# Kernel tuning notes

Hardware: AMD Instinct MI355X
Metric: run time of the kernel (lower is better)

The kernel has to match this reference:

```python
import jax, jax.numpy as jnp
import numpy as np

EPS = 1e-5        # torch BatchNorm2d default eps
G = 8             # DCNv4 groups
KP = 9            # 3x3 kernel points


def conv2d(x, w):
    return jax.lax.conv_general_dilated(
        x, w, window_strides=(1, 1), padding='SAME',
        dimension_numbers=('NCHW', 'OIHW', 'NCHW'))


def bn_eval(x, g_, b_, m_, v_):
    s = g_ / jnp.sqrt(v_ + EPS)
    return x * s[None, :, None, None] + (b_ - m_ * s)[None, :, None, None]


def silu(x):
    return x * jax.nn.sigmoid(x)


def dcnv4_core(value, offset, mask):
    # value: (N,H,W,G,Cg)  offset: (N,H,W,G,K,2) (x,y)  mask: (N,H,W,G,K) unnormalized (DCNv4: no softmax)
    N, H, W, Gn, Cg = value.shape
    r = jnp.arange(-1, 2, dtype=value.dtype)              # dilation=1, pad=1, 3x3 grid
    gy, gx = jnp.meshgrid(r, r, indexing='ij')
    grid_x = gx.ravel()  # (9,)
    grid_y = gy.ravel()
    px = jnp.arange(W, dtype=value.dtype)[None, None, :, None, None] + grid_x + offset[..., 0]
    py = jnp.arange(H, dtype=value.dtype)[None, :, None, None, None] + grid_y + offset[..., 1]
    x0 = jnp.floor(px); y0 = jnp.floor(py)
    lx = px - x0; ly = py - y0
    x0i = x0.astype(jnp.int32); y0i = y0.astype(jnp.int32)
    bidx = jnp.arange(N)[:, None, None, None, None]
    gidx = jnp.arange(Gn)[None, None, None, :, None]

    def tap(yi, xi, wgt):
        valid = (yi >= 0) & (yi < H) & (xi >= 0) & (xi < W)   # zero padding outside
        v = value[bidx, jnp.clip(yi, 0, H - 1), jnp.clip(xi, 0, W - 1), gidx]  # (N,H,W,G,K,Cg)
        return v * (wgt * valid)[..., None]

    s = (tap(y0i, x0i, (1 - ly) * (1 - lx))
         + tap(y0i, x0i + 1, (1 - ly) * lx)
         + tap(y0i + 1, x0i, ly * (1 - lx))
         + tap(y0i + 1, x0i + 1, ly * lx))
    return jnp.einsum('nhwgkc,nhwgk->nhwgc', s, mask)


def dcnv4(x, val_w, val_b, om_w, om_b, outp_w, outp_b):
    # x: NCHW. DCNv4 wrapper: flatten to tokens, value_proj, offset_mask linear on raw tokens,
    # deformable aggregation, output_proj, back to NCHW.
    N, C, H, W = x.shape
    t = x.transpose(0, 2, 3, 1).reshape(N, H * W, C)
    value = (t @ val_w.T + val_b).reshape(N, H, W, G, C // G)
    om = (t @ om_w.T + om_b).reshape(N, H, W, G, KP * 3)  # per group: 2K offsets then K masks
    offset = om[..., :2 * KP].reshape(N, H, W, G, KP, 2)
    mask = om[..., 2 * KP:]
    out = dcnv4_core(value, offset, mask).reshape(N, H * W, C)
    out = out @ outp_w.T + outp_b
    return out.reshape(N, H, W, C).transpose(0, 3, 1, 2)


def setup_inputs() -> dict:
    key = jax.random.key(0)
    ks = jax.random.split(key, 32)
    W_SC = 0.05
    d = {}
    d['x'] = jax.random.normal(ks[0], (4, 256, 64, 64), jnp.float32)
    d['cv1_w'] = jax.random.normal(ks[1], (128, 256, 3, 3), jnp.float32) * W_SC
    d['cv1_bn_g'] = jax.random.uniform(ks[2], (128,), jnp.float32, 0.5, 1.5)
    d['cv1_bn_b'] = jax.random.normal(ks[3], (128,), jnp.float32) * 0.1
    d['cv1_bn_m'] = jax.random.normal(ks[4], (128,), jnp.float32) * 0.1
    d['cv1_bn_v'] = jax.random.uniform(ks[5], (128,), jnp.float32, 0.5, 1.5)
    d['cv2_w'] = jax.random.normal(ks[6], (256, 128, 3, 3), jnp.float32) * W_SC
    d['cv2_bn_g'] = jax.random.uniform(ks[7], (256,), jnp.float32, 0.5, 1.5)
    d['cv2_bn_b'] = jax.random.normal(ks[8], (256,), jnp.float32) * 0.1
    d['cv2_bn_m'] = jax.random.normal(ks[9], (256,), jnp.float32) * 0.1
    d['cv2_bn_v'] = jax.random.uniform(ks[10], (256,), jnp.float32, 0.5, 1.5)
    d['val_w'] = jax.random.normal(ks[11], (256, 256), jnp.float32) * W_SC
    d['val_b'] = jax.random.normal(ks[12], (256,), jnp.float32) * 0.01
    d['om_w'] = jax.random.normal(ks[13], (216, 256), jnp.float32) * 0.02
    d['om_b'] = jax.random.normal(ks[14], (216,), jnp.float32) * 0.01
    d['outp_w'] = jax.random.normal(ks[15], (256, 256), jnp.float32) * W_SC
    d['outp_b'] = jax.random.normal(ks[16], (256,), jnp.float32) * 0.01
    d['bn3_g'] = jax.random.uniform(ks[17], (256,), jnp.float32, 0.5, 1.5)
    d['bn3_b'] = jax.random.normal(ks[18], (256,), jnp.float32) * 0.1
    d['bn3_m'] = jax.random.normal(ks[19], (256,), jnp.float32) * 0.1
    d['bn3_v'] = jax.random.uniform(ks[20], (256,), jnp.float32, 0.5, 1.5)
    d['pw1_w'] = jax.random.normal(ks[21], (768, 256, 1, 1), jnp.float32) * W_SC
    d['pw1_b'] = jax.random.normal(ks[22], (768,), jnp.float32) * 0.01
    d['pw2_w'] = jax.random.normal(ks[23], (256, 768, 1, 1), jnp.float32) * W_SC
    d['pw2_b'] = jax.random.normal(ks[24], (256,), jnp.float32) * 0.01
    return d


def reference(x, cv1_w, cv1_bn_g, cv1_bn_b, cv1_bn_m, cv1_bn_v,
              cv2_w, cv2_bn_g, cv2_bn_b, cv2_bn_m, cv2_bn_v,
              val_w, val_b, om_w, om_b, outp_w, outp_b,
              bn3_g, bn3_b, bn3_m, bn3_v, pw1_w, pw1_b, pw2_w, pw2_b):
    # cv2(cv1(x)) branch: Conv = Conv2d(no bias) + BN + SiLU
    y = silu(bn_eval(conv2d(x, cv1_w), cv1_bn_g, cv1_bn_b, cv1_bn_m, cv1_bn_v))
    y = silu(bn_eval(conv2d(y, cv2_w), cv2_bn_g, cv2_bn_b, cv2_bn_m, cv2_bn_v))
    # dcn branch: DCNv4 -> BN -> 1x1 conv (+SiLU) -> 1x1 conv
    d = dcnv4(x, val_w, val_b, om_w, om_b, outp_w, outp_b)
    d = bn_eval(d, bn3_g, bn3_b, bn3_m, bn3_v)
    d = silu(conv2d(d, pw1_w) + pw1_b[None, :, None, None])
    d = conv2d(d, pw2_w) + pw2_b[None, :, None, None]
    return x + y + d
```

## Files before the change

### kernel.cpp

```cpp
#include <hip/hip_runtime.h>
#include <math.h>

typedef __attribute__((ext_vector_type(8))) __bf16 bf16x8;
typedef __attribute__((ext_vector_type(8))) unsigned short us8;
typedef __attribute__((ext_vector_type(4))) unsigned short us4;
typedef __attribute__((ext_vector_type(4))) float f32x4;
typedef __attribute__((ext_vector_type(4))) int i32x4;
typedef unsigned int uint32;

#define EPSV 1e-5f

__device__ __forceinline__ float silu_f(float v) { return v / (1.f + __expf(-v)); }

__device__ __forceinline__ unsigned short f2bf(float f) {
  uint32 u = __builtin_bit_cast(uint32, f);
  u += 0x7fffu + ((u >> 16) & 1u);
  return (unsigned short)(u >> 16);
}
__device__ __forceinline__ float bf2f(unsigned short h) {
  uint32 u = ((uint32)h) << 16;
  return __builtin_bit_cast(float, u);
}

__device__ __forceinline__ void gl_lds16(const void* g, void* l) {
  __builtin_amdgcn_global_load_lds(
      (const __attribute__((address_space(1))) unsigned int*)g,
      (__attribute__((address_space(3))) unsigned int*)l, 16, 0, 0);
}

template <int EPI, int CIN, int BN>
__device__ __forceinline__ void gemm_body(
    int rb, int cb, int k0, int KL,
    const unsigned short* __restrict__ A, const unsigned short* __restrict__ Bw,
    const float* __restrict__ bias, int K, int Co, void* __restrict__ outv,
    const float* __restrict__ e0, const float* __restrict__ e1,
    const float* __restrict__ e2, const float* __restrict__ e3,
    const unsigned short* __restrict__ zpage, bf16x8* smem) {
  constexpr int NFR = BN / 32;
  constexpr int NB = BN / 64;
  constexpr int CPB = 512 + BN * 4;
  const int t = threadIdx.x;
  const int lane = t & 63;
  const int wv = t >> 6;
  const int wr = wv >> 1, wc = wv & 1;

  f32x4 acc[4][NFR];
#pragma unroll
  for (int i = 0; i < 4; i++)
#pragma unroll
    for (int j = 0; j < NFR; j++) acc[i][j] = (f32x4){0.f, 0.f, 0.f, 0.f};

  const unsigned short* Abase[2];
  int aprow[2], apcol[2], akoff[2];
#pragma unroll
  for (int i = 0; i < 2; i++) {
    int c = t + 256 * i;
    int row = (c >> 6) * 16 + (c & 15);
    int koff = ((c >> 4) & 3) * 8;
    akoff[i] = koff;
    int grow = rb + row;
    if constexpr (CIN > 0) {
      int n = grow >> 12, p = grow & 4095;
      aprow[i] = p >> 6;
      apcol[i] = p & 63;
      Abase[i] = A + (size_t)n * 4096 * CIN;
    } else {
      Abase[i] = A + (size_t)grow * K + koff;
    }
  }
  const unsigned short* Bbase[NB];
#pragma unroll
  for (int i = 0; i < NB; i++) {
    int c = t + 256 * i;
    int col = cb + (c >> 6) * 16 + (c & 15);
    int koff = ((c >> 4) & 3) * 8;
    Bbase[i] = (col < Co) ? (Bw + (size_t)col * K + koff) : zpage;
  }
  auto addrA = [&](int i, int kb) -> const unsigned short* {
    if constexpr (CIN > 0) {
      int tap = kb / CIN;
      int ci = (kb & (CIN - 1)) + akoff[i];
      int dy = tap / 3 - 1, dx = tap % 3 - 1;
      int h = aprow[i] + dy, w = apcol[i] + dx;
      if (((unsigned)h < 64u) & ((unsigned)w < 64u))
        return &Abase[i][(size_t)(h * 64 + w) * CIN + ci];
      return zpage;
    } else {
      return Abase[i] + kb;
    }
  };
  auto stage = [&](int buf, int kb) {
    bf16x8* base = &smem[buf * CPB];
    gl_lds16(addrA(0, kb), (void*)&base[t]);
    gl_lds16(addrA(1, kb), (void*)&base[t + 256]);
    gl_lds16((Bbase[0] == zpage) ? zpage : Bbase[0] + kb, (void*)&base[512 + t]);
    if constexpr (NB == 2)
      gl_lds16((Bbase[1] == zpage) ? zpage : Bbase[1] + kb,
               (void*)&base[512 + t + 256]);
  };

  const int nt = KL >> 5;
  stage(0, k0);
  __syncthreads();
  int cur = 0;
  for (int it = 0; it < nt; ++it) {
    if (it + 1 < nt) stage(cur ^ 1, k0 + ((it + 1) << 5));
    const bf16x8* Ab = &smem[cur * CPB];
    const bf16x8* Bb = Ab + 512;
    bf16x8 af[4], bfr[NFR];
#pragma unroll
    for (int mi = 0; mi < 4; mi++) af[mi] = Ab[(wr * 4 + mi) * 64 + lane];
#pragma unroll
    for (int ni = 0; ni < NFR; ni++) bfr[ni] = Bb[(wc * NFR + ni) * 64 + lane];
    __builtin_amdgcn_s_setprio(1);
#pragma unroll
    for (int mi = 0; mi < 4; mi++)
#pragma unroll
      for (int ni = 0; ni < NFR; ni++)
        acc[mi][ni] = __builtin_amdgcn_mfma_f32_16x16x32_bf16(af[mi], bfr[ni],
                                                              acc[mi][ni], 0, 0, 0);
    __builtin_amdgcn_s_setprio(0);
    __syncthreads();
    cur ^= 1;
  }

  const int lr = lane & 15, kg4 = (lane >> 4) * 4;
#pragma unroll
  for (int mi = 0; mi < 4; mi++) {
#pragma unroll
    for (int ni = 0; ni < NFR; ni++) {
      int gcol = cb + wc * (BN / 2) + ni * 16 + lr;
      if (gcol >= Co) continue;
      float bval, s = 1.f, tt = 0.f;
      if (EPI == 2 || EPI == 7) bval = 0.f;
      else if (EPI == 5) bval = (gcol < 256) ? bias[gcol] : e0[gcol - 256];
      else bval = bias[gcol];
      if (EPI == 2 || EPI == 3) {
        s = e0[gcol] * rsqrtf(e3[gcol] + EPSV);
        tt = e1[gcol] - e2[gcol] * s;
      }
      if (EPI == 6) {
        int grow0 = rb + wr * 64 + mi * 16 + kg4;
        int n = grow0 >> 12, p0 = grow0 & 4095;
        size_t oix = ((size_t)(n * 256 + gcol)) * 4096 + p0;
        f32x4 xv = *(const f32x4*)&((const float*)e0)[oix];
        const unsigned short* y2p = (const unsigned short*)e1;
        f32x4 ov;
#pragma unroll
        for (int j = 0; j < 4; j++) {
          float y2 = bf2f(y2p[((size_t)(n * 4096 + p0 + j)) * 256 + gcol]);
          ov[j] = acc[mi][ni][j] + bval + xv[j] + y2;
        }
        *(f32x4*)&((float*)outv)[oix] = ov;
        continue;
      }
#pragma unroll
      for (int j = 0; j < 4; j++) {
        int grow = rb + wr * 64 + mi * 16 + kg4 + j;
        float v = acc[mi][ni][j] + bval;
        if (EPI == 2) v = silu_f(v * s + tt);
        if (EPI == 3) v = v * s + tt;
        if (EPI == 4) v = silu_f(v);
        if (EPI == 5) {
          if (gcol < 256)
            ((unsigned short*)outv)[(size_t)grow * 256 + gcol] = f2bf(v);
          else
            ((float*)e1)[(size_t)grow * 216 + (gcol - 256)] = v;
        } else {
          ((unsigned short*)outv)[(size_t)grow * Co + gcol] = f2bf(v);
        }
      }
    }
  }
}

__device__ __forceinline__ void dcn_body(
    int bid, const unsigned short* __restrict__ value,
    const float* __restrict__ om, unsigned short* __restrict__ out,
    void* smemraw) {
  f32x4* wgt = (f32x4*)smemraw;
  i32x4* adr = (i32x4*)((char*)smemraw + 576 * 16);
  const int n = bid >> 9;
  const int p0 = (bid & 511) * 8;
  const int t = threadIdx.x;

  for (int idx = t; idx < 576; idx += 256) {
    int pi = idx / 72;
    int gk = idx - pi * 72;
    int g = gk / 9, k = gk - g * 9;
    int p = p0 + pi;
    int h0 = p >> 6, w0 = p & 63;
    const float* omp = om + ((size_t)(n * 4096 + p)) * 216 + g * 27;
    float ox = omp[2 * k], oy = omp[2 * k + 1], mk = omp[18 + k];
    float px = (float)(w0 + (k % 3) - 1) + ox;
    float py = (float)(h0 + (k / 3) - 1) + oy;
    float x0f = floorf(px), y0f = floorf(py);
    float lx = px - x0f, ly = py - y0f;
    int x0 = (int)x0f, y0 = (int)y0f;
    int x1 = x0 + 1, y1 = y0 + 1;
    bool vx0 = (unsigned)x0 < 64u, vx1 = (unsigned)x1 < 64u;
    bool vy0 = (unsigned)y0 < 64u, vy1 = (unsigned)y1 < 64u;
    int cx0 = min(max(x0, 0), 63), cx1 = min(max(x1, 0), 63);
    int cy0 = min(max(y0, 0), 63), cy1 = min(max(y1, 0), 63);
    f32x4 w4;
    w4[0] = (1.f - ly) * (1.f - lx) * mk * (float)(vy0 && vx0);
    w4[1] = (1.f - ly) * lx * mk * (float)(vy0 && vx1);
    w4[2] = ly * (1.f - lx) * mk * (float)(vy1 && vx0);
    w4[3] = ly * lx * mk * (float)(vy1 && vx1);
    i32x4 a4;
    a4[0] = (cy0 * 64 + cx0) * 256;
    a4[1] = (cy0 * 64 + cx1) * 256;
    a4[2] = (cy1 * 64 + cx0) * 256;
    a4[3] = (cy1 * 64 + cx1) * 256;
    wgt[idx] = w4;
    adr[idx] = a4;
  }
  __syncthreads();

  const int pi = t >> 5;
  const int g = (t >> 2) & 7;
  const int l = t & 3;
  const int p = p0 + pi;
  const unsigned short* vb = value + ((size_t)n * 4096) * 256 + g * 32 + l * 8;
  const int bix = (pi * 8 + g) * 9;
  float a[8] = {0.f, 0.f, 0.f, 0.f, 0.f, 0.f, 0.f, 0.f};
#pragma unroll
  for (int k = 0; k < 9; k++) {
    f32x4 wv = wgt[bix + k];
    i32x4 av = adr[bix + k];
    us8 q0 = *(const us8*)(vb + av[0]);
    us8 q1 = *(const us8*)(vb + av[1]);
    us8 q2 = *(const us8*)(vb + av[2]);
    us8 q3 = *(const us8*)(vb + av[3]);
#pragma unroll
    for (int j = 0; j < 8; j++)
      a[j] += wv[0] * bf2f(q0[j]) + wv[1] * bf2f(q1[j]) +
              wv[2] * bf2f(q2[j]) + wv[3] * bf2f(q3[j]);
  }
  us8 o;
#pragma unroll
  for (int j = 0; j < 8; j++) o[j] = f2bf(a[j]);
  *(us8*)&out[((size_t)(n * 4096 + p)) * 256 + g * 32 + l * 8] = o;
}

__global__ __launch_bounds__(256) void prep_k(
    const float* __restrict__ x, unsigned short* __restrict__ xt,
    const float* __restrict__ c1, unsigned short* __restrict__ o1,
    const float* __restrict__ c2, unsigned short* __restrict__ o2,
    const float* __restrict__ a0, unsigned short* __restrict__ b0,
    const float* __restrict__ a1, unsigned short* __restrict__ b1,
    const float* __restrict__ a2, unsigned short* __restrict__ b2,
    const float* __restrict__ a3, unsigned short* __restrict__ b3,
    const float* __restrict__ a4, unsigned short* __restrict__ b4,
    uint32* __restrict__ zp) {
  __shared__ float lds[64][65];
  int b = blockIdx.x;
  const int t = threadIdx.x;
  if (b == 0 && t < 32) zp[t] = 0u;
  if (b < 1024) {
    const int p0 = (b & 63) * 64, c0 = ((b >> 6) & 3) * 64, n = b >> 8;
    const int pp = t & 63, ccb = t >> 6;
    const float* xb = x + ((size_t)n * 256 + c0) * 4096 + p0;
#pragma unroll
    for (int i = 0; i < 16; i++) {
      int cc = ccb * 16 + i;
      lds[pp][cc] = xb[(size_t)cc * 4096 + pp];
    }
    __syncthreads();
#pragma unroll
    for (int i = 0; i < 2; i++) {
      int pp2 = (t >> 3) + i * 32;
      int c8 = (t & 7) * 8;
      us8 v;
#pragma unroll
      for (int j = 0; j < 8; j++) v[j] = f2bf(lds[pp2][c8 + j]);
      *(us8*)&xt[((size_t)(n * 4096 + p0 + pp2)) * 256 + c0 + c8] = v;
    }
    return;
  }
  if (b < 1152) {
    int idx = (b - 1024) * 256 + t;
    int co = idx >> 8, ci = idx & 255;
    const float* src = c1 + (size_t)(co * 256 + ci) * 9;
#pragma unroll
    for (int tap = 0; tap < 9; tap++)
      o1[(size_t)(co * 9 + tap) * 256 + ci] = f2bf(src[tap]);
    return;
  }
  if (b < 1280) {
    int idx = (b - 1152) * 256 + t;
    int co = idx >> 7, ci = idx & 127;
    const float* src = c2 + (size_t)(co * 128 + ci) * 9;
#pragma unroll
    for (int tap = 0; tap < 9; tap++)
      o2[(size_t)(co * 9 + tap) * 128 + ci] = f2bf(src[tap]);
    return;
  }
  int idx = (b - 1280) * 256 + t;
  const float* s;
  unsigned short* d;
  int off;
  if (idx < 65536)       { s = a0; d = b0; off = idx; }
  else if (idx < 120832) { s = a1; d = b1; off = idx - 65536; }
  else if (idx < 186368) { s = a2; d = b2; off = idx - 120832; }
  else if (idx < 382976) { s = a3; d = b3; off = idx - 186368; }
  else if (idx < 579584) { s = a4; d = b4; off = idx - 382976; }
  else return;
  d[off] = f2bf(s[off]);
}

__global__ __launch_bounds__(256) void fused_s1(
    const unsigned short* __restrict__ xt,
    const unsigned short* __restrict__ wc1, unsigned short* __restrict__ part,
    const unsigned short* __restrict__ wval, const float* __restrict__ val_b,
    const float* __restrict__ om_b, float* __restrict__ omf,
    unsigned short* __restrict__ valt, const unsigned short* __restrict__ zpage) {
  __shared__ bf16x8 smem[2048];
  int b = blockIdx.x;
  if (b < 512) {
    int s = b >> 7, mt = b & 127;
    gemm_body<7, 256, 128>(mt * 128, 0, s * 576, 576, xt, wc1, nullptr, 2304,
                           128, part + (size_t)s * 2097152, nullptr, nullptr,
                           nullptr, nullptr, zpage, smem);
  } else {
    b -= 512;
    gemm_body<5, 0, 128>((b >> 2) * 128, (b & 3) * 128, 0, 256, xt, wval, val_b,
                         256, 472, valt, om_b, (const float*)omf, nullptr,
                         nullptr, zpage, smem);
  }
}

__global__ __launch_bounds__(256) void fused_r(
    const unsigned short* __restrict__ part, const float* __restrict__ g1,
    const float* __restrict__ bb1, const float* __restrict__ m1,
    const float* __restrict__ v1, unsigned short* __restrict__ y1t,
    const unsigned short* __restrict__ valt, const float* __restrict__ omf,
    unsigned short* __restrict__ dcnt) {
  __shared__ char rsm[18432];
  int b = blockIdx.x;
  if (b < 1024) {
    int g = b * 256 + threadIdx.x;
    int grow = g >> 4;
    int co8 = (g & 15) << 3;
    size_t base = (size_t)grow * 128 + co8;
    float sum[8] = {0.f, 0.f, 0.f, 0.f, 0.f, 0.f, 0.f, 0.f};
#pragma unroll
    for (int s = 0; s < 4; s++) {
      us8 pv = *(const us8*)&part[base + (size_t)s * 2097152];
#pragma unroll
      for (int j = 0; j < 8; j++) sum[j] += bf2f(pv[j]);
    }
    us8 o;
#pragma unroll
    for (int j = 0; j < 8; j++) {
      int co = co8 + j;
      float sc = g1[co] * rsqrtf(v1[co] + EPSV);
      float tt = bb1[co] - m1[co] * sc;
      o[j] = f2bf(silu_f(sum[j] * sc + tt));
    }
    *(us8*)&y1t[base] = o;
  } else {
    dcn_body(b - 1024, valt, omf, dcnt, (void*)rsm);
  }
}

__global__ __launch_bounds__(256) void fused_s2(
    const unsigned short* __restrict__ y1t,
    const unsigned short* __restrict__ wc2, const float* __restrict__ g2,
    const float* __restrict__ bb2, const float* __restrict__ m2,
    const float* __restrict__ v2, unsigned short* __restrict__ y2t,
    const unsigned short* __restrict__ dcnt, const unsigned short* __restrict__ woutp,
    const float* __restrict__ outp_b, const float* __restrict__ g3,
    const float* __restrict__ bb3, const float* __restrict__ m3,
    const float* __restrict__ v3, unsigned short* __restrict__ d1t,
    const unsigned short* __restrict__ zpage) {
  __shared__ bf16x8 smem[1536];
  int b = blockIdx.x;
  if (b < 512) {
    gemm_body<2, 128, 64>((b >> 2) * 128, (b & 3) * 64, 0, 1152, y1t, wc2,
                          nullptr, 1152, 256, y2t, g2, bb2, m2, v2, zpage, smem);
  } else {
    b -= 512;
    gemm_body<3, 0, 64>((b >> 2) * 128, (b & 3) * 64, 0, 256, dcnt, woutp,
                        outp_b, 256, 256, d1t, g3, bb3, m3, v3, zpage, smem);
  }
}

template <int EPI, int CIN, int BN>
__global__ __launch_bounds__(256) void gemm_k(
    const unsigned short* __restrict__ A, const unsigned short* __restrict__ Bw,
    const float* __restrict__ bias, int K, int Co, void* __restrict__ outv,
    const float* __restrict__ e0, const float* __restrict__ e1,
    const float* __restrict__ e2, const float* __restrict__ e3,
    const unsigned short* __restrict__ zpage) {
  __shared__ bf16x8 smem[2 * (512 + BN * 4)];
  gemm_body<EPI, CIN, BN>(blockIdx.y * 128, blockIdx.x * BN, 0, K, A, Bw, bias,
                          K, Co, outv, e0, e1, e2, e3, zpage, smem);
}

extern "C" void kernel_launch(void* const* d_in, const int* in_sizes, int n_in,
                              void* d_out, int out_size, void* d_ws,
                              size_t ws_size, hipStream_t stream) {
  const float* x      = (const float*)d_in[0];
  const float* cv1_w  = (const float*)d_in[1];
  const float* cv1_g  = (const float*)d_in[2];
  const float* cv1_b  = (const float*)d_in[3];
  const float* cv1_m  = (const float*)d_in[4];
  const float* cv1_v  = (const float*)d_in[5];
  const float* cv2_w  = (const float*)d_in[6];
  const float* cv2_g  = (const float*)d_in[7];
  const float* cv2_b  = (const float*)d_in[8];
  const float* cv2_m  = (const float*)d_in[9];
  const float* cv2_v  = (const float*)d_in[10];
  const float* val_w  = (const float*)d_in[11];
  const float* val_b  = (const float*)d_in[12];
  const float* om_w   = (const float*)d_in[13];
  const float* om_b   = (const float*)d_in[14];
  const float* outp_w = (const float*)d_in[15];
  const float* outp_b = (const float*)d_in[16];
  const float* bn3_g  = (const float*)d_in[17];
  const float* bn3_b  = (const float*)d_in[18];
  const float* bn3_m  = (const float*)d_in[19];
  const float* bn3_v  = (const float*)d_in[20];
  const float* pw1_w  = (const float*)d_in[21];
  const float* pw1_b  = (const float*)d_in[22];
  const float* pw2_w  = (const float*)d_in[23];
  const float* pw2_b  = (const float*)d_in[24];
  float* out = (float*)d_out;

  char* w = (char*)d_ws;
  auto alloc = [&](size_t bytes) {
    char* p = w;
    w += (bytes + 255) & ~(size_t)255;
    return p;
  };
  unsigned short* xt    = (unsigned short*)alloc(16384ull * 256 * 2);
  unsigned short* y1t   = (unsigned short*)alloc(16384ull * 128 * 2);
  unsigned short* y2t   = (unsigned short*)alloc(16384ull * 256 * 2);
  unsigned short* valt  = (unsigned short*)alloc(16384ull * 256 * 2);
  float*          omf   = (float*)alloc(16384ull * 216 * 4);
  unsigned short* dcnt  = (unsigned short*)alloc(16384ull * 256 * 2);
  unsigned short* d1t   = (unsigned short*)alloc(16384ull * 256 * 2);
  unsigned short* p1t   = (unsigned short*)alloc(16384ull * 768 * 2);
  unsigned short* part = d1t;
  unsigned short* wc1   = (unsigned short*)alloc(128ull * 2304 * 2);
  unsigned short* wc2   = (unsigned short*)alloc(256ull * 1152 * 2);
  unsigned short* wval  = (unsigned short*)alloc(256ull * 256 * 2);
  unsigned short* wom   = (unsigned short*)alloc(216ull * 256 * 2);
  unsigned short* woutp = (unsigned short*)alloc(256ull * 256 * 2);
  unsigned short* wpw1  = (unsigned short*)alloc(768ull * 256 * 2);
  unsigned short* wpw2  = (unsigned short*)alloc(256ull * 768 * 2);
  unsigned short* zpage = (unsigned short*)alloc(256);

  prep_k<<<3544, 256, 0, stream>>>(x, xt, cv1_w, wc1, cv2_w, wc2, val_w, wval,
                                   om_w, wom, outp_w, woutp, pw1_w, wpw1,
                                   pw2_w, wpw2, (uint32*)zpage);

  fused_s1<<<1024, 256, 0, stream>>>(xt, wc1, part, wval, val_b, om_b, omf,
                                     valt, zpage);

  fused_r<<<3072, 256, 0, stream>>>(part, cv1_g, cv1_b, cv1_m, cv1_v, y1t,
                                    valt, omf, dcnt);

  fused_s2<<<1024, 256, 0, stream>>>(y1t, wc2, cv2_g, cv2_b, cv2_m, cv2_v, y2t,
                                     dcnt, woutp, outp_b, bn3_g, bn3_b, bn3_m,
                                     bn3_v, d1t, zpage);

  gemm_k<4, 0, 128><<<dim3(6, 128), 256, 0, stream>>>(
      d1t, wpw1, pw1_b, 256, 768, p1t, nullptr, nullptr, nullptr, nullptr, zpage);
  gemm_k<6, 0, 64><<<dim3(4, 128), 256, 0, stream>>>(
      p1t, wpw2, pw2_b, 768, 256, out, x, (const float*)y2t, nullptr, nullptr, zpage);
}
```

Baseline: 158.8 us.

## Stage GEMM epilogue through swizzled LDS and rebalance cv2/pw1 across launches

Bf16-output GEMM epilogues now write results into a bank-swizzled LDS tile, synchronize, and then store full rows with 16-byte vector writes, replacing scattered 2-byte global stores. The cv2 3x3 GEMM blocks are also split: 320 run with the outp GEMM and the other 192 move into a new fused kernel alongside the pw1 GEMM. This aims to coalesce output writes and to balance work across kernel launches so the GPU is better filled. The cost is an extra barrier and LDS round trip per block, plus more shared memory in the fused pw1 kernel. The old bounds check on gcol against Co is dropped on the LDS path.

```diff
diff --git a/kernel.cpp b/kernel.cpp
--- a/kernel.cpp
+++ b/kernel.cpp
@@ -125,20 +125,56 @@
   }
 
   const int lr = lane & 15, kg4 = (lane >> 4) * 4;
-#pragma unroll
-  for (int mi = 0; mi < 4; mi++) {
+
+  if constexpr (EPI == 0 || EPI == 2 || EPI == 3 || EPI == 4 || EPI == 7) {
+    unsigned short* lsm = (unsigned short*)smem;
 #pragma unroll
     for (int ni = 0; ni < NFR; ni++) {
-      int gcol = cb + wc * (BN / 2) + ni * 16 + lr;
-      if (gcol >= Co) continue;
-      float bval, s = 1.f, tt = 0.f;
-      if (EPI == 2 || EPI == 7) bval = 0.f;
-      else if (EPI == 5) bval = (gcol < 256) ? bias[gcol] : e0[gcol - 256];
-      else bval = bias[gcol];
+      int lcol = wc * (BN / 2) + ni * 16 + lr;
+      int gcol = cb + lcol;
+      float bval = (EPI == 2 || EPI == 7) ? 0.f : bias[gcol];
+      float s = 1.f, tt = 0.f;
       if (EPI == 2 || EPI == 3) {
         s = e0[gcol] * rsqrtf(e3[gcol] + EPSV);
         tt = e1[gcol] - e2[gcol] * s;
       }
+#pragma unroll
+      for (int mi = 0; mi < 4; mi++) {
+#pragma unroll
+        for (int j = 0; j < 4; j++) {
+          int r = wr * 64 + mi * 16 + kg4 + j;
+          float v = acc[mi][ni][j] + bval;
+          if (EPI == 2) v = silu_f(v * s + tt);
+          if (EPI == 3) v = v * s + tt;
+          if (EPI == 4) v = silu_f(v);
+          lsm[r * BN + (lcol ^ ((((r) >> 2) & 3) << 3))] = f2bf(v);
+        }
+      }
+    }
+    __syncthreads();
+    constexpr int CPR = BN / 8;
+    constexpr int NPT = BN / 16;
+    unsigned short* outp = (unsigned short*)outv;
+#pragma unroll
+    for (int i = 0; i < NPT; i++) {
+      int chunk = i * 256 + t;
+      int r = chunk / CPR;
+      int c8 = chunk % CPR;
+      us8 v = *(const us8*)&lsm[r * BN + ((c8 ^ ((r >> 2) & 3)) * 8)];
+      *(us8*)&outp[(size_t)(rb + r) * Co + cb + c8 * 8] = v;
+    }
+    return;
+  }
+
+#pragma unroll
+  for (int mi = 0; mi < 4; mi++) {
+#pragma unroll
+    for (int ni = 0; ni < NFR; ni++) {
+      int gcol = cb + wc * (BN / 2) + ni * 16 + lr;
+      if (gcol >= Co) continue;
+      float bval;
+      if (EPI == 5) bval = (gcol < 256) ? bias[gcol] : e0[gcol - 256];
+      else bval = bias[gcol];
       if (EPI == 6) {
         int grow0 = rb + wr * 64 + mi * 16 + kg4;
         int n = grow0 >> 12, p0 = grow0 & 4095;
@@ -158,16 +194,11 @@
       for (int j = 0; j < 4; j++) {
         int grow = rb + wr * 64 + mi * 16 + kg4 + j;
         float v = acc[mi][ni][j] + bval;
-        if (EPI == 2) v = silu_f(v * s + tt);
-        if (EPI == 3) v = v * s + tt;
-        if (EPI == 4) v = silu_f(v);
         if (EPI == 5) {
           if (gcol < 256)
             ((unsigned short*)outv)[(size_t)grow * 256 + gcol] = f2bf(v);
           else
             ((float*)e1)[(size_t)grow * 216 + (gcol - 256)] = v;
-        } else {
-          ((unsigned short*)outv)[(size_t)grow * Co + gcol] = f2bf(v);
         }
       }
     }
@@ -376,13 +407,35 @@
     const unsigned short* __restrict__ zpage) {
   __shared__ bf16x8 smem[1536];
   int b = blockIdx.x;
-  if (b < 512) {
+  if (b < 320) {
     gemm_body<2, 128, 64>((b >> 2) * 128, (b & 3) * 64, 0, 1152, y1t, wc2,
                           nullptr, 1152, 256, y2t, g2, bb2, m2, v2, zpage, smem);
   } else {
-    b -= 512;
+    b -= 320;
     gemm_body<3, 0, 64>((b >> 2) * 128, (b & 3) * 64, 0, 256, dcnt, woutp,
                         outp_b, 256, 256, d1t, g3, bb3, m3, v3, zpage, smem);
+  }
+}
+
+__global__ __launch_bounds__(256) void fused_p1(
+    const unsigned short* __restrict__ y1t,
+    const unsigned short* __restrict__ wc2, const float* __restrict__ g2,
+    const float* __restrict__ bb2, const float* __restrict__ m2,
+    const float* __restrict__ v2, unsigned short* __restrict__ y2t,
+    const unsigned short* __restrict__ d1t, const unsigned short* __restrict__ wpw1,
+    const float* __restrict__ pw1_b, unsigned short* __restrict__ p1t,
+    const unsigned short* __restrict__ zpage) {
+  __shared__ bf16x8 smem[2048];
+  int b = blockIdx.x;
+  if (b < 192) {
+    int c = b + 320;
+    gemm_body<2, 128, 64>((c >> 2) * 128, (c & 3) * 64, 0, 1152, y1t, wc2,
+                          nullptr, 1152, 256, y2t, g2, bb2, m2, v2, zpage, smem);
+  } else {
+    b -= 192;
+    gemm_body<4, 0, 128>((b / 6) * 128, (b % 6) * 128, 0, 256, d1t, wpw1,
+                         pw1_b, 256, 768, p1t, nullptr, nullptr, nullptr,
+                         nullptr, zpage, smem);
   }
 }
 
@@ -462,12 +515,13 @@
   fused_r<<<3072, 256, 0, stream>>>(part, cv1_g, cv1_b, cv1_m, cv1_v, y1t,
                                     valt, omf, dcnt);
 
-  fused_s2<<<1024, 256, 0, stream>>>(y1t, wc2, cv2_g, cv2_b, cv2_m, cv2_v, y2t,
-                                     dcnt, woutp, outp_b, bn3_g, bn3_b, bn3_m,
-                                     bn3_v, d1t, zpage);
-
-  gemm_k<4, 0, 128><<<dim3(6, 128), 256, 0, stream>>>(
-      d1t, wpw1, pw1_b, 256, 768, p1t, nullptr, nullptr, nullptr, nullptr, zpage);
+  fused_s2<<<832, 256, 0, stream>>>(y1t, wc2, cv2_g, cv2_b, cv2_m, cv2_v, y2t,
+                                    dcnt, woutp, outp_b, bn3_g, bn3_b, bn3_m,
+                                    bn3_v, d1t, zpage);
+
+  fused_p1<<<960, 256, 0, stream>>>(y1t, wc2, cv2_g, cv2_b, cv2_m, cv2_v, y2t,
+                                    d1t, wpw1, pw1_b, p1t, zpage);
+
   gemm_k<6, 0, 64><<<dim3(4, 128), 256, 0, stream>>>(
       p1t, wpw2, pw2_b, 768, 256, out, x, (const float*)y2t, nullptr, nullptr, zpage);
 }
```

Result: slower. 166.5 us (+4.8%).

## Use 128x64 tiles with BK=64 in all GEMMs and double block counts

Applied to the files above, without the earlier changes.

Replaces the templated GEMM body with one fixed 128x64 output tile that stages 64-wide K slices, doing two MFMA k-steps per barrier. This halves the number of LDS sync iterations. The cv1, value/offset and pw1 GEMMs move from 128-wide to 64-wide column tiles, which doubles their grid sizes for more parallelism. In exchange it uses more LDS per block (48KB), which may lower occupancy, and loads the A tile redundantly across column tiles.

```diff
diff --git a/kernel.cpp b/kernel.cpp
--- a/kernel.cpp
+++ b/kernel.cpp
@@ -28,35 +28,33 @@
       (__attribute__((address_space(3))) unsigned int*)l, 16, 0, 0);
 }
 
-template <int EPI, int CIN, int BN>
-__device__ __forceinline__ void gemm_body(
+template <int EPI, int CIN>
+__device__ __forceinline__ void gemm_body64(
     int rb, int cb, int k0, int KL,
     const unsigned short* __restrict__ A, const unsigned short* __restrict__ Bw,
     const float* __restrict__ bias, int K, int Co, void* __restrict__ outv,
     const float* __restrict__ e0, const float* __restrict__ e1,
     const float* __restrict__ e2, const float* __restrict__ e3,
     const unsigned short* __restrict__ zpage, bf16x8* smem) {
-  constexpr int NFR = BN / 32;
-  constexpr int NB = BN / 64;
-  constexpr int CPB = 512 + BN * 4;
+  constexpr int CPB = 1536;
   const int t = threadIdx.x;
   const int lane = t & 63;
   const int wv = t >> 6;
   const int wr = wv >> 1, wc = wv & 1;
 
-  f32x4 acc[4][NFR];
+  f32x4 acc[4][2];
 #pragma unroll
   for (int i = 0; i < 4; i++)
 #pragma unroll
-    for (int j = 0; j < NFR; j++) acc[i][j] = (f32x4){0.f, 0.f, 0.f, 0.f};
-
-  const unsigned short* Abase[2];
-  int aprow[2], apcol[2], akoff[2];
-#pragma unroll
-  for (int i = 0; i < 2; i++) {
+    for (int j = 0; j < 2; j++) acc[i][j] = (f32x4){0.f, 0.f, 0.f, 0.f};
+
+  const unsigned short* Abase[4];
+  int aprow[4], apcol[4], akoff[4];
+#pragma unroll
+  for (int i = 0; i < 4; i++) {
     int c = t + 256 * i;
-    int row = (c >> 6) * 16 + (c & 15);
-    int koff = ((c >> 4) & 3) * 8;
+    int row = (c >> 7) * 16 + (c & 15);
+    int koff = ((c >> 6) & 1) * 32 + ((c >> 4) & 3) * 8;
     akoff[i] = koff;
     int grow = rb + row;
     if constexpr (CIN > 0) {
@@ -68,12 +66,12 @@
       Abase[i] = A + (size_t)grow * K + koff;
     }
   }
-  const unsigned short* Bbase[NB];
-#pragma unroll
-  for (int i = 0; i < NB; i++) {
+  const unsigned short* Bbase[2];
+#pragma unroll
+  for (int i = 0; i < 2; i++) {
     int c = t + 256 * i;
-    int col = cb + (c >> 6) * 16 + (c & 15);
-    int koff = ((c >> 4) & 3) * 8;
+    int col = cb + (c >> 7) * 16 + (c & 15);
+    int koff = ((c >> 6) & 1) * 32 + ((c >> 4) & 3) * 8;
     Bbase[i] = (col < Co) ? (Bw + (size_t)col * K + koff) : zpage;
   }
   auto addrA = [&](int i, int kb) -> const unsigned short* {
@@ -91,34 +89,40 @@
   };
   auto stage = [&](int buf, int kb) {
     bf16x8* base = &smem[buf * CPB];
-    gl_lds16(addrA(0, kb), (void*)&base[t]);
-    gl_lds16(addrA(1, kb), (void*)&base[t + 256]);
-    gl_lds16((Bbase[0] == zpage) ? zpage : Bbase[0] + kb, (void*)&base[512 + t]);
-    if constexpr (NB == 2)
-      gl_lds16((Bbase[1] == zpage) ? zpage : Bbase[1] + kb,
-               (void*)&base[512 + t + 256]);
+#pragma unroll
+    for (int i = 0; i < 4; i++)
+      gl_lds16(addrA(i, kb), (void*)&base[t + 256 * i]);
+    gl_lds16((Bbase[0] == zpage) ? zpage : Bbase[0] + kb,
+             (void*)&base[1024 + t]);
+    gl_lds16((Bbase[1] == zpage) ? zpage : Bbase[1] + kb,
+             (void*)&base[1024 + t + 256]);
   };
 
-  const int nt = KL >> 5;
+  const int nt = KL >> 6;
   stage(0, k0);
   __syncthreads();
   int cur = 0;
   for (int it = 0; it < nt; ++it) {
-    if (it + 1 < nt) stage(cur ^ 1, k0 + ((it + 1) << 5));
+    if (it + 1 < nt) stage(cur ^ 1, k0 + ((it + 1) << 6));
     const bf16x8* Ab = &smem[cur * CPB];
-    const bf16x8* Bb = Ab + 512;
-    bf16x8 af[4], bfr[NFR];
-#pragma unroll
-    for (int mi = 0; mi < 4; mi++) af[mi] = Ab[(wr * 4 + mi) * 64 + lane];
-#pragma unroll
-    for (int ni = 0; ni < NFR; ni++) bfr[ni] = Bb[(wc * NFR + ni) * 64 + lane];
+    const bf16x8* Bb = Ab + 1024;
     __builtin_amdgcn_s_setprio(1);
 #pragma unroll
-    for (int mi = 0; mi < 4; mi++)
-#pragma unroll
-      for (int ni = 0; ni < NFR; ni++)
-        acc[mi][ni] = __builtin_amdgcn_mfma_f32_16x16x32_bf16(af[mi], bfr[ni],
-                                                              acc[mi][ni], 0, 0, 0);
+    for (int ks = 0; ks < 2; ks++) {
+      bf16x8 af[4], bfr[2];
+#pragma unroll
+      for (int mi = 0; mi < 4; mi++)
+        af[mi] = Ab[((wr * 4 + mi) * 2 + ks) * 64 + lane];
+#pragma unroll
+      for (int ni = 0; ni < 2; ni++)
+        bfr[ni] = Bb[((wc * 2 + ni) * 2 + ks) * 64 + lane];
+#pragma unroll
+      for (int mi = 0; mi < 4; mi++)
+#pragma unroll
+        for (int ni = 0; ni < 2; ni++)
+          acc[mi][ni] = __builtin_amdgcn_mfma_f32_16x16x32_bf16(
+              af[mi], bfr[ni], acc[mi][ni], 0, 0, 0);
+    }
     __builtin_amdgcn_s_setprio(0);
     __syncthreads();
     cur ^= 1;
@@ -128,8 +132,8 @@
 #pragma unroll
   for (int mi = 0; mi < 4; mi++) {
 #pragma unroll
-    for (int ni = 0; ni < NFR; ni++) {
-      int gcol = cb + wc * (BN / 2) + ni * 16 + lr;
+    for (int ni = 0; ni < 2; ni++) {
+      int gcol = cb + wc * 32 + ni * 16 + lr;
       if (gcol >= Co) continue;
       float bval, s = 1.f, tt = 0.f;
       if (EPI == 2 || EPI == 7) bval = 0.f;
@@ -315,18 +319,19 @@
     const unsigned short* __restrict__ wval, const float* __restrict__ val_b,
     const float* __restrict__ om_b, float* __restrict__ omf,
     unsigned short* __restrict__ valt, const unsigned short* __restrict__ zpage) {
-  __shared__ bf16x8 smem[2048];
+  __shared__ bf16x8 smem[3072];
   int b = blockIdx.x;
-  if (b < 512) {
-    int s = b >> 7, mt = b & 127;
-    gemm_body<7, 256, 128>(mt * 128, 0, s * 576, 576, xt, wc1, nullptr, 2304,
-                           128, part + (size_t)s * 2097152, nullptr, nullptr,
-                           nullptr, nullptr, zpage, smem);
+  if (b < 1024) {
+    int s = b >> 8, c = b & 255;
+    int mt = c >> 1, ct = c & 1;
+    gemm_body64<7, 256>(mt * 128, ct * 64, s * 576, 576, xt, wc1, nullptr,
+                        2304, 128, part + (size_t)s * 2097152, nullptr,
+                        nullptr, nullptr, nullptr, zpage, smem);
   } else {
-    b -= 512;
-    gemm_body<5, 0, 128>((b >> 2) * 128, (b & 3) * 128, 0, 256, xt, wval, val_b,
-                         256, 472, valt, om_b, (const float*)omf, nullptr,
-                         nullptr, zpage, smem);
+    int v = b - 1024;
+    gemm_body64<5, 0>((v >> 3) * 128, (v & 7) * 64, 0, 256, xt, wval, val_b,
+                      256, 472, valt, om_b, (const float*)omf, nullptr,
+                      nullptr, zpage, smem);
   }
 }
 
@@ -374,28 +379,29 @@
     const float* __restrict__ bb3, const float* __restrict__ m3,
     const float* __restrict__ v3, unsigned short* __restrict__ d1t,
     const unsigned short* __restrict__ zpage) {
-  __shared__ bf16x8 smem[1536];
+  __shared__ bf16x8 smem[3072];
   int b = blockIdx.x;
   if (b < 512) {
-    gemm_body<2, 128, 64>((b >> 2) * 128, (b & 3) * 64, 0, 1152, y1t, wc2,
-                          nullptr, 1152, 256, y2t, g2, bb2, m2, v2, zpage, smem);
+    gemm_body64<2, 128>((b >> 2) * 128, (b & 3) * 64, 0, 1152, y1t, wc2,
+                        nullptr, 1152, 256, y2t, g2, bb2, m2, v2, zpage, smem);
   } else {
     b -= 512;
-    gemm_body<3, 0, 64>((b >> 2) * 128, (b & 3) * 64, 0, 256, dcnt, woutp,
-                        outp_b, 256, 256, d1t, g3, bb3, m3, v3, zpage, smem);
-  }
-}
-
-template <int EPI, int CIN, int BN>
-__global__ __launch_bounds__(256) void gemm_k(
+    gemm_body64<3, 0>((b >> 2) * 128, (b & 3) * 64, 0, 256, dcnt, woutp,
+                      outp_b, 256, 256, d1t, g3, bb3, m3, v3, zpage, smem);
+  }
+}
+
+template <int EPI, int NCB>
+__global__ __launch_bounds__(256) void gemm_k64(
     const unsigned short* __restrict__ A, const unsigned short* __restrict__ Bw,
     const float* __restrict__ bias, int K, int Co, void* __restrict__ outv,
     const float* __restrict__ e0, const float* __restrict__ e1,
     const float* __restrict__ e2, const float* __restrict__ e3,
     const unsigned short* __restrict__ zpage) {
-  __shared__ bf16x8 smem[2 * (512 + BN * 4)];
-  gemm_body<EPI, CIN, BN>(blockIdx.y * 128, blockIdx.x * BN, 0, K, A, Bw, bias,
-                          K, Co, outv, e0, e1, e2, e3, zpage, smem);
+  __shared__ bf16x8 smem[3072];
+  int b = blockIdx.x;
+  gemm_body64<EPI, 0>((b / NCB) * 128, (b % NCB) * 64, 0, K, A, Bw, bias,
+                      K, Co, outv, e0, e1, e2, e3, zpage, smem);
 }
 
 extern "C" void kernel_launch(void* const* d_in, const int* in_sizes, int n_in,
@@ -456,7 +462,7 @@
                                    om_w, wom, outp_w, woutp, pw1_w, wpw1,
                                    pw2_w, wpw2, (uint32*)zpage);
 
-  fused_s1<<<1024, 256, 0, stream>>>(xt, wc1, part, wval, val_b, om_b, omf,
+  fused_s1<<<2048, 256, 0, stream>>>(xt, wc1, part, wval, val_b, om_b, omf,
                                      valt, zpage);
 
   fused_r<<<3072, 256, 0, stream>>>(part, cv1_g, cv1_b, cv1_m, cv1_v, y1t,
@@ -466,8 +472,8 @@
                                      dcnt, woutp, outp_b, bn3_g, bn3_b, bn3_m,
                                      bn3_v, d1t, zpage);
 
-  gemm_k<4, 0, 128><<<dim3(6, 128), 256, 0, stream>>>(
+  gemm_k64<4, 12><<<1536, 256, 0, stream>>>(
       d1t, wpw1, pw1_b, 256, 768, p1t, nullptr, nullptr, nullptr, nullptr, zpage);
-  gemm_k<6, 0, 64><<<dim3(4, 128), 256, 0, stream>>>(
+  gemm_k64<6, 4><<<512, 256, 0, stream>>>(
       p1t, wpw2, pw2_b, 768, 256, out, x, (const float*)y2t, nullptr, nullptr, zpage);
 }
```

Measured after the change: 169.6 us. 1.07x slower.
